# Optimization experiments

Hardware: AMD Instinct MI355X
Metric: run time of the kernel (lower is better)

## Reference

```python
import jax, jax.numpy as jnp
import numpy as np

N_NODES = 50000
N_EDGES = 600000
NFEAT = 256
NHID = 128
NCLASS = 40


def setup_inputs() -> dict:
    key = jax.random.key(0)
    ks = jax.random.split(key, 10)
    x = jax.random.normal(ks[0], (N_NODES, NFEAT), dtype=jnp.float32)
    edge_src = jax.random.randint(ks[1], (N_EDGES,), 0, N_NODES, dtype=jnp.int32)
    edge_dst = jax.random.randint(ks[2], (N_EDGES,), 0, N_NODES, dtype=jnp.int32)
    # normalized adjacency weights (positive, ~1/deg scale)
    edge_weight = jax.random.uniform(ks[3], (N_EDGES,), dtype=jnp.float32) * 0.2
    # GraphConvolution params (Glorot-ish init)
    W1 = jax.random.normal(ks[4], (NFEAT, NHID), dtype=jnp.float32) / np.float32(np.sqrt(NFEAT))
    b1 = jnp.zeros((NHID,), dtype=jnp.float32)
    W2 = jax.random.normal(ks[5], (NHID, NHID), dtype=jnp.float32) / np.float32(np.sqrt(NHID))
    b2 = jnp.zeros((NHID,), dtype=jnp.float32)
    W3 = jax.random.normal(ks[6], (NHID, NCLASS), dtype=jnp.float32) / np.float32(np.sqrt(NHID))
    b3 = jnp.zeros((NCLASS,), dtype=jnp.float32)
    return {"x": x, "edge_weight": edge_weight, "W1": W1, "b1": b1,
            "W2": W2, "b2": b2, "W3": W3, "b3": b3,
            "edge_src": edge_src, "edge_dst": edge_dst}


def _gcn_layer(h, W, b, edge_src, edge_dst, edge_weight):
    # support = h @ W ; out = spmm(adj, support) + b
    support = h @ W                                   # [N, out]
    msgs = support[edge_src] * edge_weight[:, None]   # [E, out]
    agg = jax.ops.segment_sum(msgs, edge_dst, num_segments=N_NODES)
    return agg + b


def reference(x, edge_weight, W1, b1, W2, b2, W3, b3, edge_src, edge_dst):
    # eval mode: F.dropout(training=False) is identity
    h = jax.nn.relu(_gcn_layer(x, W1, b1, edge_src, edge_dst, edge_weight))
    h = jax.nn.relu(_gcn_layer(h, W2, b2, edge_src, edge_dst, edge_weight))
    h = _gcn_layer(h, W3, b3, edge_src, edge_dst, edge_weight)
    return jax.nn.log_softmax(h, axis=1)
```

## Files before the change

### kernel.cpp

```cpp
#include <hip/hip_runtime.h>
#include <math.h>

#define N_NODES 50000
#define N_EDGES 600000
#define NFEAT   256
#define NHID    128
#define NCLASS  40
#define NBUCK 196
#define EPB_A 2048
#define BUCK_CAP 4096
#define BUCK_WIN 5888
#define BINA_BLOCKS ((N_EDGES + EPB_A - 1) / EPB_A)
#define CVTW_BLOCKS 224
#define GEMM_BLOCKS ((N_NODES + 63) / 64)
#define TILE_BLOCKS ((N_NODES + 31) / 32)

typedef __attribute__((ext_vector_type(8))) short bf16x8;
typedef __attribute__((ext_vector_type(4))) float f32x4;
typedef __attribute__((ext_vector_type(2))) float f32x2;

__device__ inline ushort f2bf(float f) {
    uint u = __float_as_uint(f);
    uint r = (u + 0x7fffu + ((u >> 16) & 1u)) >> 16;
    return (ushort)r;
}

__global__ __launch_bounds__(256) void binA_cvtw(const int* __restrict__ src,
                                                 const int* __restrict__ dst,
                                                 const float* __restrict__ w,
                                                 int* __restrict__ bucket_cnt,
                                                 int2* __restrict__ staging, int E,
                                                 const float* __restrict__ W1,
                                                 const float* __restrict__ W2,
                                                 const float* __restrict__ W3,
                                                 ushort* __restrict__ BT1,
                                                 ushort* __restrict__ BT2,
                                                 ushort* __restrict__ BT3) {
    int tid = threadIdx.x;
    if ((int)blockIdx.x >= BINA_BLOCKS) {
        int idx = ((int)blockIdx.x - BINA_BLOCKS) * 256 + tid;
        if (idx < 32768) {
            int nr = idx >> 8, k = idx & 255;
            BT1[idx] = f2bf(W1[(size_t)k * 128 + nr]);
        } else if (idx < 49152) {
            int t = idx - 32768;
            int nr = t >> 7, k = t & 127;
            BT2[t] = f2bf(W2[(size_t)k * 128 + nr]);
        } else if (idx < 57344) {
            int t = idx - 49152;
            int nr = t >> 7, k = t & 127;
            BT3[t] = (nr < 40) ? f2bf(W3[(size_t)k * 40 + nr]) : (ushort)0;
        }
        return;
    }
    __shared__ int lh[NBUCK];
    for (int b = tid; b < NBUCK; b += 256) lh[b] = 0;
    __syncthreads();
    int base = blockIdx.x * EPB_A;
    int d[8];
    #pragma unroll
    for (int j = 0; j < 8; ++j) {
        int i = base + j * 256 + tid;
        d[j] = (i < E) ? dst[i] : -1;
        if (d[j] >= 0) atomicAdd(&lh[d[j] >> 8], 1);
    }
    __syncthreads();
    for (int b = tid; b < NBUCK; b += 256) {
        int c = lh[b];
        lh[b] = c ? (b * BUCK_CAP + atomicAdd(&bucket_cnt[b], c)) : 0;
    }
    __syncthreads();
    #pragma unroll
    for (int j = 0; j < 8; ++j) {
        int i = base + j * 256 + tid;
        if (d[j] >= 0) {
            int slot = atomicAdd(&lh[d[j] >> 8], 1);
            uint rec = ((uint)f2bf(w[i]) << 16) | (uint)src[i];
            staging[slot] = make_int2((int)rec, d[j] & 255);
        }
    }
}

template<int NT, bool AF32>
__device__ __forceinline__ void gemm_body(const void* __restrict__ Ain,
                                          const ushort* __restrict__ BT,
                                          int M, int K, int Nout,
                                          ushort* __restrict__ Cout, int row0) {
    __shared__ ushort a_s[64 * 40];
    __shared__ ushort b_s[64 * NT * 40];
    int tid = threadIdx.x;
    int wave = tid >> 6, lane = tid & 63;
    int lr = lane & 15, lk = (lane >> 4) * 8;
    f32x4 acc[4][NT];
    #pragma unroll
    for (int mt = 0; mt < 4; ++mt)
        #pragma unroll
        for (int nt = 0; nt < NT; ++nt) acc[mt][nt] = (f32x4){0.f, 0.f, 0.f, 0.f};

    for (int k0 = 0; k0 < K; k0 += 32) {
        {
            int r = tid >> 2, c8 = (tid & 3) * 8;
            int gr = row0 + r; if (gr >= M) gr = M - 1;
            if (AF32) {
                const float* Af = (const float*)Ain;
                float4 v0 = *(const float4*)(Af + (size_t)gr * K + k0 + c8);
                float4 v1 = *(const float4*)(Af + (size_t)gr * K + k0 + c8 + 4);
                ushort4 o0, o1;
                o0.x = f2bf(v0.x); o0.y = f2bf(v0.y); o0.z = f2bf(v0.z); o0.w = f2bf(v0.w);
                o1.x = f2bf(v1.x); o1.y = f2bf(v1.y); o1.z = f2bf(v1.z); o1.w = f2bf(v1.w);
                *(ushort4*)(a_s + r * 40 + c8) = o0;
                *(ushort4*)(a_s + r * 40 + c8 + 4) = o1;
            } else {
                const ushort* Ab = (const ushort*)Ain;
                float4 v = *(const float4*)(Ab + (size_t)gr * K + k0 + c8);
                *(float4*)(a_s + r * 40 + c8) = v;
            }
        }
        #pragma unroll
        for (int i = 0; i < NT; ++i) {
            int idx = tid * NT + i;
            int r = idx >> 2, c8 = (idx & 3) * 8;
            float4 v = *(const float4*)(BT + (size_t)r * K + k0 + c8);
            *(float4*)(b_s + r * 40 + c8) = v;
        }
        __syncthreads();
        bf16x8 bfr[NT];
        #pragma unroll
        for (int nt = 0; nt < NT; ++nt)
            bfr[nt] = *(const bf16x8*)(b_s + ((wave * NT + nt) * 16 + lr) * 40 + lk);
        #pragma unroll
        for (int mt = 0; mt < 4; ++mt) {
            bf16x8 afr = *(const bf16x8*)(a_s + (mt * 16 + lr) * 40 + lk);
            #pragma unroll
            for (int nt = 0; nt < NT; ++nt)
                acc[mt][nt] = __builtin_amdgcn_mfma_f32_16x16x32_bf16(
                    afr, bfr[nt], acc[mt][nt], 0, 0, 0);
        }
        __syncthreads();
    }
    int col0 = wave * NT * 16;
    #pragma unroll
    for (int mt = 0; mt < 4; ++mt) {
        int gr0 = row0 + mt * 16 + (lane >> 4) * 4;
        #pragma unroll
        for (int nt = 0; nt < NT; ++nt) {
            int gc = col0 + nt * 16 + lr;
            #pragma unroll
            for (int i = 0; i < 4; ++i) {
                int gr = gr0 + i;
                if (gr < M && gc < Nout)
                    Cout[(size_t)gr * Nout + gc] = f2bf(acc[mt][nt][i]);
            }
        }
    }
}

__global__ __launch_bounds__(256) void scan_gemm1(const int* __restrict__ bucket_cnt,
                                                  const int2* __restrict__ staging,
                                                  int2* __restrict__ rsp2,
                                                  uint* __restrict__ edges,
                                                  const float* __restrict__ x,
                                                  const ushort* __restrict__ BT1,
                                                  ushort* __restrict__ supA) {
    if ((int)blockIdx.x >= NBUCK) {
        gemm_body<2, true>(x, BT1, N_NODES, 256, 128, supA,
                           ((int)blockIdx.x - NBUCK) * 64);
        return;
    }
    __shared__ int hist[256];
    __shared__ int buf[256];
    __shared__ int lcur[256];
    int tid = threadIdx.x;
    hist[tid] = 0;
    __syncthreads();
    int b = blockIdx.x;
    int c = bucket_cnt[b];
    const int2* st = staging + (size_t)b * BUCK_CAP;
    for (int p = tid; p < c; p += 256) atomicAdd(&hist[st[p].y], 1);
    __syncthreads();
    int v = (hist[tid] + 7) & ~7;
    buf[tid] = v;
    __syncthreads();
    #pragma unroll
    for (int off = 1; off < 256; off <<= 1) {
        int t = (tid >= off) ? buf[tid - off] : 0;
        __syncthreads();
        buf[tid] += t;
        __syncthreads();
    }
    int bb = b * BUCK_WIN;
    int ex = buf[tid] - v + bb;
    int i = b * 256 + tid;
    if (i < N_NODES) rsp2[i] = make_int2(ex, ex + v);
    lcur[tid] = ex;
    __syncthreads();
    int e0 = bb + buf[255];
    for (int p = bb + tid; p < e0; p += 256) edges[p] = 0;
    __syncthreads();
    for (int p = tid; p < c; p += 256) {
        int2 r = st[p];
        int slot = atomicAdd(&lcur[r.y], 1);
        edges[slot] = (uint)r.x;
    }
}


#define LDREC_S(R, POS) do { \
    int _ub = __builtin_amdgcn_readfirstlane(POS); \
    _Pragma("unroll") \
    for (int _i = 0; _i < 16; ++_i) R[_i] = edges[_ub + _i]; \
} while (0)

#define GATHER_S(P, R) do { \
    _Pragma("unroll") \
    for (int _j = 0; _j < 16; ++_j) { \
        uint _idx = R[_j] & 0xffffu; \
        _idx = (_idx < N_NODES) ? _idx : (N_NODES - 1);   \
        P[_j] = sup[(size_t)_idx * 64 + lane]; \
    } \
} while (0)

#define FLUSH_A() do { \
    uint _pk = ((uint)f2bf(fmaxf(acc2.y + by, 0.f)) << 16) \
             |  (uint)f2bf(fmaxf(acc2.x + bx, 0.f)); \
    *(uint*)(&a4_s[ks][(wave * 8 + cur) * 40 + kk]) = _pk; \
    acc2 = (f32x2){0.f, 0.f}; \
    ++cur; \
    e_cur = (cur < 8) ? e_s[wave][cur + 1] : 0x7fffffff; \
} while (0)

#define FMA_A(QB, P, R) do { \
    _Pragma("unroll") \
    for (int _g = 0; _g < 2; ++_g) { \
        int _qg = (QB) + _g * 8; \
        while (cur < 8 && _qg >= e_cur) FLUSH_A(); \
        if (_qg < QE) { \
            _Pragma("unroll") \
            for (int _j = 0; _j < 8; ++_j) { \
                uint _pv = P[_g * 8 + _j]; \
                float _w = __uint_as_float(R[_g * 8 + _j] & 0xffff0000u); \
                f32x2 _v; \
                _v.x = __uint_as_float(_pv << 16); \
                _v.y = __uint_as_float(_pv & 0xffff0000u); \
                acc2 += _v * (f32x2){_w, _w}; \
            } \
        } \
    } \
} while (0)

template<int NT>
__device__ __forceinline__ void fused_body(const uint* __restrict__ sup,
                                           const int2* __restrict__ rsp2,
                                           const uint* __restrict__ edges,
                                           const float* __restrict__ bias,
                                           const ushort* __restrict__ BT,
                                           int Nout,
                                           ushort* __restrict__ Cout) {
    __shared__ ushort a4_s[4][32 * 40];
    __shared__ int e_s[4][9];
    int tid = threadIdx.x;
    int wave = tid >> 6, lane = tid & 63;
    int row0 = blockIdx.x * 32;
    int nfirst = row0 + wave * 8;
    float bx = bias[2 * lane], by = bias[2 * lane + 1];
    int ks = lane >> 4;
    int kk = 2 * (lane & 15);

    if (lane < 8) {
        int nd = nfirst + lane; if (nd >= N_NODES) nd = N_NODES - 1;
        int2 t = rsp2[nd];
        e_s[wave][lane + 1] = t.y;
        if (lane == 0) e_s[wave][0] = t.x;
    }
    __syncthreads();
    int Q = e_s[wave][0], QE = e_s[wave][8];
    int cur = 0, e_cur = e_s[wave][1];
    f32x2 acc2 = (f32x2){0.f, 0.f};

    uint ra[16], rb[16], rc[16];
    uint pa[16], pb[16];
    int q = Q;
    LDREC_S(ra, q);
    GATHER_S(pa, ra);
    LDREC_S(rb, q + 16);
    while (q < QE) {
        GATHER_S(pb, rb); LDREC_S(rc, q + 32); FMA_A(q, pa, ra);
        q += 16; if (q >= QE) break;
        GATHER_S(pa, rc); LDREC_S(ra, q + 32); FMA_A(q, pb, rb);
        q += 16; if (q >= QE) break;
        GATHER_S(pb, ra); LDREC_S(rb, q + 32); FMA_A(q, pa, rc);
        q += 16; if (q >= QE) break;
        GATHER_S(pa, rb); LDREC_S(rc, q + 32); FMA_A(q, pb, ra);
        q += 16; if (q >= QE) break;
        GATHER_S(pb, rc); LDREC_S(ra, q + 32); FMA_A(q, pa, rb);
        q += 16; if (q >= QE) break;
        GATHER_S(pa, ra); LDREC_S(rb, q + 32); FMA_A(q, pb, rc);
        q += 16;
    }
    while (cur < 8) FLUSH_A();
    __syncthreads();

    int lr = lane & 15, lk = (lane >> 4) * 8;
    f32x4 acc[2][NT];
    #pragma unroll
    for (int mt = 0; mt < 2; ++mt)
        #pragma unroll
        for (int nt = 0; nt < NT; ++nt) acc[mt][nt] = (f32x4){0.f, 0.f, 0.f, 0.f};
    #pragma unroll
    for (int ksi = 0; ksi < 4; ++ksi) {
        int k0 = ksi * 32;
        bf16x8 bfr[NT];
        #pragma unroll
        for (int nt = 0; nt < NT; ++nt)
            bfr[nt] = *(const bf16x8*)(BT +
                (size_t)((wave * NT + nt) * 16 + lr) * 128 + k0 + lk);
        #pragma unroll
        for (int mt = 0; mt < 2; ++mt) {
            bf16x8 afr = *(const bf16x8*)(&a4_s[ksi][(mt * 16 + lr) * 40 + lk]);
            #pragma unroll
            for (int nt = 0; nt < NT; ++nt)
                acc[mt][nt] = __builtin_amdgcn_mfma_f32_16x16x32_bf16(
                    afr, bfr[nt], acc[mt][nt], 0, 0, 0);
        }
    }
    int col0 = wave * NT * 16;
    #pragma unroll
    for (int mt = 0; mt < 2; ++mt) {
        int gr0 = row0 + mt * 16 + (lane >> 4) * 4;
        #pragma unroll
        for (int nt = 0; nt < NT; ++nt) {
            int gc = col0 + nt * 16 + lr;
            #pragma unroll
            for (int i = 0; i < 4; ++i) {
                int gr = gr0 + i;
                if (gr < N_NODES && gc < Nout)
                    Cout[(size_t)gr * Nout + gc] = f2bf(acc[mt][nt][i]);
            }
        }
    }
}

__global__ __launch_bounds__(256) void fused_ag2(const uint* __restrict__ sup,
                                                 const int2* __restrict__ rsp2,
                                                 const uint* __restrict__ edges,
                                                 const float* __restrict__ bias,
                                                 const ushort* __restrict__ BT,
                                                 ushort* __restrict__ Cout) {
    fused_body<2>(sup, rsp2, edges, bias, BT, 128, Cout);
}

__global__ __launch_bounds__(256) void fused_ag3(const uint* __restrict__ sup,
                                                 const int2* __restrict__ rsp2,
                                                 const uint* __restrict__ edges,
                                                 const float* __restrict__ bias,
                                                 const ushort* __restrict__ BT,
                                                 ushort* __restrict__ Cout) {
    fused_body<1>(sup, rsp2, edges, bias, BT, 64, Cout);
}


#define GATHER_L(P, R) do { \
    _Pragma("unroll") \
    for (int _j = 0; _j < 16; ++_j) { \
        uint _idx = R[_j] & 0xffffu; \
        _idx = (_idx < N_NODES) ? _idx : (N_NODES - 1); \
        P[_j] = __uint_as_float((uint)sup[(size_t)_idx * 64 + lane] << 16); \
    } \
} while (0)

#define FLUSH_L() do { \
    int _node = nfirst + cur; \
    float _v = (lane < 40) ? acc1 + bl : -INFINITY; \
    float _m = _v; \
    _Pragma("unroll") \
    for (int _o = 32; _o; _o >>= 1) _m = fmaxf(_m, __shfl_xor(_m, _o, 64)); \
    float _ex = (lane < 40) ? expf(_v - _m) : 0.f; \
    float _s = _ex; \
    _Pragma("unroll") \
    for (int _o = 32; _o; _o >>= 1) _s += __shfl_xor(_s, _o, 64); \
    float _ls = logf(_s); \
    if (lane < 40 && _node < N_NODES) \
        out[(size_t)_node * 40 + lane] = _v - _m - _ls; \
    acc1 = 0.f; \
    ++cur; \
    e_cur = (cur < 8) ? e_s[wave][cur + 1] : 0x7fffffff; \
} while (0)

#define FMA_L(QB, P, R) do { \
    _Pragma("unroll") \
    for (int _g = 0; _g < 2; ++_g) { \
        int _qg = (QB) + _g * 8; \
        while (cur < 8 && _qg >= e_cur) FLUSH_L(); \
        if (_qg < QE) { \
            _Pragma("unroll") \
            for (int _j = 0; _j < 8; ++_j) \
                acc1 += P[_g * 8 + _j] * \
                        __uint_as_float(R[_g * 8 + _j] & 0xffff0000u); \
        } \
    } \
} while (0)

__global__ __launch_bounds__(256) void agg_lsm(const ushort* __restrict__ sup,
                                               const int2* __restrict__ rsp2,
                                               const uint* __restrict__ edges,
                                               const float* __restrict__ bias,
                                               float* __restrict__ out) {
    __shared__ int e_s[4][9];
    int tid = threadIdx.x;
    int wave = tid >> 6, lane = tid & 63;
    int nfirst = blockIdx.x * 32 + wave * 8;
    float bl = (lane < 40) ? bias[lane] : 0.f;
    if (lane < 8) {
        int nd = nfirst + lane; if (nd >= N_NODES) nd = N_NODES - 1;
        int2 t = rsp2[nd];
        e_s[wave][lane + 1] = t.y;
        if (lane == 0) e_s[wave][0] = t.x;
    }
    __syncthreads();
    int Q = e_s[wave][0], QE = e_s[wave][8];
    int cur = 0, e_cur = e_s[wave][1];
    float acc1 = 0.f;

    uint ra[16], rb[16], rc[16];
    float pa[16], pb[16];
    int q = Q;
    LDREC_S(ra, q);
    GATHER_L(pa, ra);
    LDREC_S(rb, q + 16);
    while (q < QE) {
        GATHER_L(pb, rb); LDREC_S(rc, q + 32); FMA_L(q, pa, ra);
        q += 16; if (q >= QE) break;
        GATHER_L(pa, rc); LDREC_S(ra, q + 32); FMA_L(q, pb, rb);
        q += 16; if (q >= QE) break;
        GATHER_L(pb, ra); LDREC_S(rb, q + 32); FMA_L(q, pa, rc);
        q += 16; if (q >= QE) break;
        GATHER_L(pa, rb); LDREC_S(rc, q + 32); FMA_L(q, pb, ra);
        q += 16; if (q >= QE) break;
        GATHER_L(pb, rc); LDREC_S(ra, q + 32); FMA_L(q, pa, rb);
        q += 16; if (q >= QE) break;
        GATHER_L(pa, ra); LDREC_S(rb, q + 32); FMA_L(q, pb, rc);
        q += 16;
    }
    while (cur < 8) FLUSH_L();
}

extern "C" void kernel_launch(void* const* d_in, const int* in_sizes, int n_in,
                              void* d_out, int out_size, void* d_ws, size_t ws_size,
                              hipStream_t stream) {
    const float* x   = (const float*)d_in[0];
    const float* ew  = (const float*)d_in[1];
    const float* W1  = (const float*)d_in[2];
    const float* b1  = (const float*)d_in[3];
    const float* W2  = (const float*)d_in[4];
    const float* b2  = (const float*)d_in[5];
    const float* W3  = (const float*)d_in[6];
    const float* b3  = (const float*)d_in[7];
    const int* esrc  = (const int*)d_in[8];
    const int* edst  = (const int*)d_in[9];
    float* out = (float*)d_out;

    char* ws = (char*)d_ws;
    size_t off = 0;
    auto alloc = [&](size_t bytes) {
        size_t cur = off;
        off += (bytes + 255) & ~(size_t)255;
        return cur;
    };
    int* bucket_cnt = (int*)(ws + alloc(256 * sizeof(int)));
    int2* rsp2   = (int2*)(ws + alloc((size_t)N_NODES * sizeof(int2)));
    uint* edges  = (uint*)(ws + alloc((size_t)NBUCK * BUCK_WIN * sizeof(uint)));
    int2* staging = (int2*)(ws + alloc((size_t)NBUCK * BUCK_CAP * sizeof(int2)));
    ushort* BT1  = (ushort*)(ws + alloc(128 * 256 * 2));
    ushort* BT2  = (ushort*)(ws + alloc(128 * 128 * 2));
    ushort* BT3  = (ushort*)(ws + alloc(64 * 128 * 2));
    char* Sreg   = ws + alloc((size_t)N_NODES * 128 * 2);
    char* Hreg   = ws + alloc((size_t)N_NODES * 128 * 2);
    (void)alloc((size_t)66000 * 128 * 2);

    ushort* supA = (ushort*)Sreg;
    ushort* supB = (ushort*)Hreg;
    ushort* sup3 = (ushort*)Sreg;

    hipMemsetAsync(bucket_cnt, 0, 256 * sizeof(int), stream);
    binA_cvtw<<<BINA_BLOCKS + CVTW_BLOCKS, 256, 0, stream>>>(
        esrc, edst, ew, bucket_cnt, staging, N_EDGES, W1, W2, W3, BT1, BT2, BT3);
    scan_gemm1<<<NBUCK + GEMM_BLOCKS, 256, 0, stream>>>(
        bucket_cnt, staging, rsp2, edges, x, BT1, supA);
    fused_ag2<<<TILE_BLOCKS, 256, 0, stream>>>(
        (const uint*)supA, rsp2, edges, b1, BT2, supB);
    fused_ag3<<<TILE_BLOCKS, 256, 0, stream>>>(
        (const uint*)supB, rsp2, edges, b2, BT3, sup3);
    agg_lsm<<<TILE_BLOCKS, 256, 0, stream>>>(sup3, rsp2, edges, b3, out);
}
```

Before: 210.2 us.

## Deepen gather pipeline to three stages and use wave-shuffle scan in bucket prefix sum

The SpMM gather loops in the fused and final-layer kernels now keep two gathers and three index-record loads in flight instead of one gather and two loads. Four record buffers and three payload buffers rotate through a 12-step unrolled loop. The goal is to hide more of the random-access gather latency, at the cost of more registers and possibly lower occupancy. Separately, the 256-thread bucket prefix scan switches from a shared-memory Hillis-Steele loop with many barriers to wave shuffles plus a small cross-wave combine.

```diff
diff --git a/kernel.cpp b/kernel.cpp
--- a/kernel.cpp
+++ b/kernel.cpp
@@ -168,8 +168,8 @@
         return;
     }
     __shared__ int hist[256];
-    __shared__ int buf[256];
     __shared__ int lcur[256];
+    __shared__ int wsum[4];
     int tid = threadIdx.x;
     hist[tid] = 0;
     __syncthreads();
@@ -179,22 +179,26 @@
     for (int p = tid; p < c; p += 256) atomicAdd(&hist[st[p].y], 1);
     __syncthreads();
     int v = (hist[tid] + 7) & ~7;
-    buf[tid] = v;
-    __syncthreads();
-    #pragma unroll
-    for (int off = 1; off < 256; off <<= 1) {
-        int t = (tid >= off) ? buf[tid - off] : 0;
-        __syncthreads();
-        buf[tid] += t;
-        __syncthreads();
-    }
+    int lane = tid & 63, wv = tid >> 6;
+    int s = v;
+    #pragma unroll
+    for (int off = 1; off < 64; off <<= 1) {
+        int t = __shfl_up(s, off, 64);
+        if (lane >= off) s += t;
+    }
+    if (lane == 63) wsum[wv] = s;
+    __syncthreads();
+    int woff = 0;
+    #pragma unroll
+    for (int j = 0; j < 4; ++j) woff += (j < wv) ? wsum[j] : 0;
+    int tot = wsum[0] + wsum[1] + wsum[2] + wsum[3];
     int bb = b * BUCK_WIN;
-    int ex = buf[tid] - v + bb;
+    int ex = s - v + woff + bb;
     int i = b * 256 + tid;
     if (i < N_NODES) rsp2[i] = make_int2(ex, ex + v);
     lcur[tid] = ex;
     __syncthreads();
-    int e0 = bb + buf[255];
+    int e0 = bb + tot;
     for (int p = bb + tid; p < e0; p += 256) edges[p] = 0;
     __syncthreads();
     for (int p = tid; p < c; p += 256) {
@@ -247,6 +251,34 @@
         } \
     } \
 } while (0)
+
+#define PIPE12(GTH, FMA) \
+    while (q < QE) { \
+        LDREC_S(rd, q + 48); GTH(pc, rc); FMA(q, pa, ra); \
+        q += 16; if (q >= QE) break; \
+        LDREC_S(ra, q + 48); GTH(pa, rd); FMA(q, pb, rb); \
+        q += 16; if (q >= QE) break; \
+        LDREC_S(rb, q + 48); GTH(pb, ra); FMA(q, pc, rc); \
+        q += 16; if (q >= QE) break; \
+        LDREC_S(rc, q + 48); GTH(pc, rb); FMA(q, pa, rd); \
+        q += 16; if (q >= QE) break; \
+        LDREC_S(rd, q + 48); GTH(pa, rc); FMA(q, pb, ra); \
+        q += 16; if (q >= QE) break; \
+        LDREC_S(ra, q + 48); GTH(pb, rd); FMA(q, pc, rb); \
+        q += 16; if (q >= QE) break; \
+        LDREC_S(rb, q + 48); GTH(pc, ra); FMA(q, pa, rc); \
+        q += 16; if (q >= QE) break; \
+        LDREC_S(rc, q + 48); GTH(pa, rb); FMA(q, pb, rd); \
+        q += 16; if (q >= QE) break; \
+        LDREC_S(rd, q + 48); GTH(pb, rc); FMA(q, pc, ra); \
+        q += 16; if (q >= QE) break; \
+        LDREC_S(ra, q + 48); GTH(pc, rd); FMA(q, pa, rb); \
+        q += 16; if (q >= QE) break; \
+        LDREC_S(rb, q + 48); GTH(pa, ra); FMA(q, pb, rc); \
+        q += 16; if (q >= QE) break; \
+        LDREC_S(rc, q + 48); GTH(pb, rb); FMA(q, pc, rd); \
+        q += 16; \
+    }
 
 template<int NT>
 __device__ __forceinline__ void fused_body(const uint* __restrict__ sup,
@@ -277,26 +309,15 @@
     int cur = 0, e_cur = e_s[wave][1];
     f32x2 acc2 = (f32x2){0.f, 0.f};
 
-    uint ra[16], rb[16], rc[16];
-    uint pa[16], pb[16];
+    uint ra[16], rb[16], rc[16], rd[16];
+    uint pa[16], pb[16], pc[16];
     int q = Q;
     LDREC_S(ra, q);
+    LDREC_S(rb, q + 16);
+    LDREC_S(rc, q + 32);
     GATHER_S(pa, ra);
-    LDREC_S(rb, q + 16);
-    while (q < QE) {
-        GATHER_S(pb, rb); LDREC_S(rc, q + 32); FMA_A(q, pa, ra);
-        q += 16; if (q >= QE) break;
-        GATHER_S(pa, rc); LDREC_S(ra, q + 32); FMA_A(q, pb, rb);
-        q += 16; if (q >= QE) break;
-        GATHER_S(pb, ra); LDREC_S(rb, q + 32); FMA_A(q, pa, rc);
-        q += 16; if (q >= QE) break;
-        GATHER_S(pa, rb); LDREC_S(rc, q + 32); FMA_A(q, pb, ra);
-        q += 16; if (q >= QE) break;
-        GATHER_S(pb, rc); LDREC_S(ra, q + 32); FMA_A(q, pa, rb);
-        q += 16; if (q >= QE) break;
-        GATHER_S(pa, ra); LDREC_S(rb, q + 32); FMA_A(q, pb, rc);
-        q += 16;
-    }
+    GATHER_S(pb, rb);
+    PIPE12(GATHER_S, FMA_A)
     while (cur < 8) FLUSH_A();
     __syncthreads();
 
@@ -421,26 +442,15 @@
     int cur = 0, e_cur = e_s[wave][1];
     float acc1 = 0.f;
 
-    uint ra[16], rb[16], rc[16];
-    float pa[16], pb[16];
+    uint ra[16], rb[16], rc[16], rd[16];
+    float pa[16], pb[16], pc[16];
     int q = Q;
     LDREC_S(ra, q);
+    LDREC_S(rb, q + 16);
+    LDREC_S(rc, q + 32);
     GATHER_L(pa, ra);
-    LDREC_S(rb, q + 16);
-    while (q < QE) {
-        GATHER_L(pb, rb); LDREC_S(rc, q + 32); FMA_L(q, pa, ra);
-        q += 16; if (q >= QE) break;
-        GATHER_L(pa, rc); LDREC_S(ra, q + 32); FMA_L(q, pb, rb);
-        q += 16; if (q >= QE) break;
-        GATHER_L(pb, ra); LDREC_S(rb, q + 32); FMA_L(q, pa, rc);
-        q += 16; if (q >= QE) break;
-        GATHER_L(pa, rb); LDREC_S(rc, q + 32); FMA_L(q, pb, ra);
-        q += 16; if (q >= QE) break;
-        GATHER_L(pb, rc); LDREC_S(ra, q + 32); FMA_L(q, pa, rb);
-        q += 16; if (q >= QE) break;
-        GATHER_L(pa, ra); LDREC_S(rb, q + 32); FMA_L(q, pb, rc);
-        q += 16;
-    }
+    GATHER_L(pb, rb);
+    PIPE12(GATHER_L, FMA_L)
     while (cur < 8) FLUSH_L();
 }
 
```

Measured after the change: 222.1 us. 1.06x slower.

## Stage full A row-block in LDS for gemm1, use wave-shuffle scan, shrink layer-3 support width

Applied to the files above, without the earlier changes.

The first GEMM now loads and converts the whole 64x256 A tile into LDS once and reads B fragments straight from global memory. This removes the per-k-step LDS staging of B and the barriers inside the K loop. The bucket prefix scan swaps the barrier-heavy Hillis-Steele loop in shared memory for a wave-level shuffle scan plus a four-way wave-sum combine. The layer-3 support matrix is stored 40 wide instead of padded to 64, which cuts gather bytes in the final aggregation; lanes 40 and above read a clamped duplicate column. The trade-off is that B fragments now come from global or L2 without LDS reuse, and the larger LDS tile may lower occupancy.

```diff
diff --git a/kernel.cpp b/kernel.cpp
--- a/kernel.cpp
+++ b/kernel.cpp
@@ -81,75 +81,63 @@
     }
 }
 
-template<int NT, bool AF32>
-__device__ __forceinline__ void gemm_body(const void* __restrict__ Ain,
-                                          const ushort* __restrict__ BT,
-                                          int M, int K, int Nout,
-                                          ushort* __restrict__ Cout, int row0) {
-    __shared__ ushort a_s[64 * 40];
-    __shared__ ushort b_s[64 * NT * 40];
+__device__ __forceinline__ void gemm1_body(const float* __restrict__ x,
+                                           const ushort* __restrict__ BT1,
+                                           ushort* __restrict__ supA, int row0) {
+    __shared__ ushort a_s[64][264];
     int tid = threadIdx.x;
     int wave = tid >> 6, lane = tid & 63;
+    {
+        int r = tid >> 2, c0 = (tid & 3) * 64;
+        int gr = row0 + r; if (gr >= N_NODES) gr = N_NODES - 1;
+        const float* sp = x + (size_t)gr * 256 + c0;
+        #pragma unroll
+        for (int j = 0; j < 8; ++j) {
+            float4 v0 = *(const float4*)(sp + j * 8);
+            float4 v1 = *(const float4*)(sp + j * 8 + 4);
+            ushort4 o0, o1;
+            o0.x = f2bf(v0.x); o0.y = f2bf(v0.y); o0.z = f2bf(v0.z); o0.w = f2bf(v0.w);
+            o1.x = f2bf(v1.x); o1.y = f2bf(v1.y); o1.z = f2bf(v1.z); o1.w = f2bf(v1.w);
+            *(ushort4*)(&a_s[r][c0 + j * 8]) = o0;
+            *(ushort4*)(&a_s[r][c0 + j * 8 + 4]) = o1;
+        }
+    }
+    __syncthreads();
     int lr = lane & 15, lk = (lane >> 4) * 8;
-    f32x4 acc[4][NT];
+    f32x4 acc[4][2];
     #pragma unroll
     for (int mt = 0; mt < 4; ++mt)
         #pragma unroll
-        for (int nt = 0; nt < NT; ++nt) acc[mt][nt] = (f32x4){0.f, 0.f, 0.f, 0.f};
-
-    for (int k0 = 0; k0 < K; k0 += 32) {
-        {
-            int r = tid >> 2, c8 = (tid & 3) * 8;
-            int gr = row0 + r; if (gr >= M) gr = M - 1;
-            if (AF32) {
-                const float* Af = (const float*)Ain;
-                float4 v0 = *(const float4*)(Af + (size_t)gr * K + k0 + c8);
-                float4 v1 = *(const float4*)(Af + (size_t)gr * K + k0 + c8 + 4);
-                ushort4 o0, o1;
-                o0.x = f2bf(v0.x); o0.y = f2bf(v0.y); o0.z = f2bf(v0.z); o0.w = f2bf(v0.w);
-                o1.x = f2bf(v1.x); o1.y = f2bf(v1.y); o1.z = f2bf(v1.z); o1.w = f2bf(v1.w);
-                *(ushort4*)(a_s + r * 40 + c8) = o0;
-                *(ushort4*)(a_s + r * 40 + c8 + 4) = o1;
-            } else {
-                const ushort* Ab = (const ushort*)Ain;
-                float4 v = *(const float4*)(Ab + (size_t)gr * K + k0 + c8);
-                *(float4*)(a_s + r * 40 + c8) = v;
-            }
-        }
-        #pragma unroll
-        for (int i = 0; i < NT; ++i) {
-            int idx = tid * NT + i;
-            int r = idx >> 2, c8 = (idx & 3) * 8;
-            float4 v = *(const float4*)(BT + (size_t)r * K + k0 + c8);
-            *(float4*)(b_s + r * 40 + c8) = v;
-        }
-        __syncthreads();
-        bf16x8 bfr[NT];
-        #pragma unroll
-        for (int nt = 0; nt < NT; ++nt)
-            bfr[nt] = *(const bf16x8*)(b_s + ((wave * NT + nt) * 16 + lr) * 40 + lk);
+        for (int nt = 0; nt < 2; ++nt) acc[mt][nt] = (f32x4){0.f, 0.f, 0.f, 0.f};
+    #pragma unroll
+    for (int ks = 0; ks < 8; ++ks) {
+        int k0 = ks * 32;
+        bf16x8 bfr[2];
+        #pragma unroll
+        for (int nt = 0; nt < 2; ++nt)
+            bfr[nt] = *(const bf16x8*)(BT1 +
+                (size_t)((wave * 2 + nt) * 16 + lr) * 256 + k0 + lk);
         #pragma unroll
         for (int mt = 0; mt < 4; ++mt) {
-            bf16x8 afr = *(const bf16x8*)(a_s + (mt * 16 + lr) * 40 + lk);
+            bf16x8 afr = *(const bf16x8*)(&a_s[mt * 16 + lr][k0 + lk]);
             #pragma unroll
-            for (int nt = 0; nt < NT; ++nt)
+            for (int nt = 0; nt < 2; ++nt)
                 acc[mt][nt] = __builtin_amdgcn_mfma_f32_16x16x32_bf16(
                     afr, bfr[nt], acc[mt][nt], 0, 0, 0);
         }
-        __syncthreads();
-    }
-    int col0 = wave * NT * 16;
+    }
+    int col0 = wave * 32;
     #pragma unroll
     for (int mt = 0; mt < 4; ++mt) {
         int gr0 = row0 + mt * 16 + (lane >> 4) * 4;
         #pragma unroll
-        for (int nt = 0; nt < NT; ++nt) {
+        for (int nt = 0; nt < 2; ++nt) {
             int gc = col0 + nt * 16 + lr;
             #pragma unroll
             for (int i = 0; i < 4; ++i) {
                 int gr = gr0 + i;
-                if (gr < M && gc < Nout)
-                    Cout[(size_t)gr * Nout + gc] = f2bf(acc[mt][nt][i]);
+                if (gr < N_NODES)
+                    supA[(size_t)gr * 128 + gc] = f2bf(acc[mt][nt][i]);
             }
         }
     }
@@ -163,13 +151,12 @@
                                                   const ushort* __restrict__ BT1,
                                                   ushort* __restrict__ supA) {
     if ((int)blockIdx.x >= NBUCK) {
-        gemm_body<2, true>(x, BT1, N_NODES, 256, 128, supA,
-                           ((int)blockIdx.x - NBUCK) * 64);
+        gemm1_body(x, BT1, supA, ((int)blockIdx.x - NBUCK) * 64);
         return;
     }
     __shared__ int hist[256];
-    __shared__ int buf[256];
     __shared__ int lcur[256];
+    __shared__ int wsum[4];
     int tid = threadIdx.x;
     hist[tid] = 0;
     __syncthreads();
@@ -179,22 +166,26 @@
     for (int p = tid; p < c; p += 256) atomicAdd(&hist[st[p].y], 1);
     __syncthreads();
     int v = (hist[tid] + 7) & ~7;
-    buf[tid] = v;
-    __syncthreads();
-    #pragma unroll
-    for (int off = 1; off < 256; off <<= 1) {
-        int t = (tid >= off) ? buf[tid - off] : 0;
-        __syncthreads();
-        buf[tid] += t;
-        __syncthreads();
-    }
+    int lane = tid & 63, wv = tid >> 6;
+    int s = v;
+    #pragma unroll
+    for (int off = 1; off < 64; off <<= 1) {
+        int t = __shfl_up(s, off, 64);
+        if (lane >= off) s += t;
+    }
+    if (lane == 63) wsum[wv] = s;
+    __syncthreads();
+    int woff = 0;
+    #pragma unroll
+    for (int j = 0; j < 4; ++j) woff += (j < wv) ? wsum[j] : 0;
+    int tot = wsum[0] + wsum[1] + wsum[2] + wsum[3];
     int bb = b * BUCK_WIN;
-    int ex = buf[tid] - v + bb;
+    int ex = s - v + woff + bb;
     int i = b * 256 + tid;
     if (i < N_NODES) rsp2[i] = make_int2(ex, ex + v);
     lcur[tid] = ex;
     __syncthreads();
-    int e0 = bb + buf[255];
+    int e0 = bb + tot;
     for (int p = bb + tid; p < e0; p += 256) edges[p] = 0;
     __syncthreads();
     for (int p = tid; p < c; p += 256) {
@@ -355,7 +346,7 @@
                                                  const float* __restrict__ bias,
                                                  const ushort* __restrict__ BT,
                                                  ushort* __restrict__ Cout) {
-    fused_body<1>(sup, rsp2, edges, bias, BT, 64, Cout);
+    fused_body<1>(sup, rsp2, edges, bias, BT, 40, Cout);
 }
 
 
@@ -364,7 +355,7 @@
     for (int _j = 0; _j < 16; ++_j) { \
         uint _idx = R[_j] & 0xffffu; \
         _idx = (_idx < N_NODES) ? _idx : (N_NODES - 1); \
-        P[_j] = __uint_as_float((uint)sup[(size_t)_idx * 64 + lane] << 16); \
+        P[_j] = __uint_as_float((uint)sup[(size_t)_idx * 40 + lf] << 16); \
     } \
 } while (0)
 
@@ -410,6 +401,7 @@
     int wave = tid >> 6, lane = tid & 63;
     int nfirst = blockIdx.x * 32 + wave * 8;
     float bl = (lane < 40) ? bias[lane] : 0.f;
+    int lf = (lane < 40) ? lane : 39;
     if (lane < 8) {
         int nd = nfirst + lane; if (nd >= N_NODES) nd = N_NODES - 1;
         int2 t = rsp2[nd];
```

Result: slower. 214.6 us (+2.1%).
